# Kernel optimization log

Measured on AMD Instinct MI355X. Metric: run time of the kernel, lower is better.

Reference implementation:

```python
import jax, jax.numpy as jnp
import numpy as np

INC, OUTC, NHEADS, KSIZE = 256, 256, 8, 5


def setup_inputs() -> dict:
    key = jax.random.key(0)
    k1, k2 = jax.random.split(key, 2)
    x = jax.random.normal(k1, (4, INC, 64, 64), dtype=jnp.float32)
    w_qkv = jax.random.normal(k2, (3 * OUTC, INC), dtype=jnp.float32) * 0.02
    b_qkv = jnp.zeros((3 * OUTC,), dtype=jnp.float32)
    return {"x": x, "w_qkv": w_qkv, "b_qkv": b_qkv}


def reference(x, w_qkv, b_qkv):
    N, Cin, H, W = x.shape
    hd = OUTC // NHEADS
    ofs = KSIZE // 2
    K2 = KSIZE * KSIZE

    # 1x1 conv == pointwise matmul over channels
    qkv = jnp.einsum('nchw,dc->ndhw', x, w_qkv) + b_qkv[None, :, None, None]
    Q = qkv[:, :OUTC]
    K = qkv[:, OUTC:2 * OUTC]
    V = qkv[:, 2 * OUTC:]

    # Zero-pad K/V; track validity so boundary softmax only spans in-bounds
    # positions (the torch code slices smaller windows at borders -> no pad
    # contribution to softmax).
    Kp = jnp.pad(K, ((0, 0), (0, 0), (ofs, ofs), (ofs, ofs)))
    Vp = jnp.pad(V, ((0, 0), (0, 0), (ofs, ofs), (ofs, ofs)))
    valid = jnp.pad(jnp.ones((H, W), dtype=bool), ((ofs, ofs), (ofs, ofs)))

    # Sliding windows via KSIZE^2 static shifted slices: [N,D,H,W,K2]
    k_win = jnp.stack([Kp[:, :, dy:dy + H, dx:dx + W]
                       for dy in range(KSIZE) for dx in range(KSIZE)], axis=-1)
    v_win = jnp.stack([Vp[:, :, dy:dy + H, dx:dx + W]
                       for dy in range(KSIZE) for dx in range(KSIZE)], axis=-1)
    m_win = jnp.stack([valid[dy:dy + H, dx:dx + W]
                       for dy in range(KSIZE) for dx in range(KSIZE)], axis=-1)  # [H,W,K2]

    qh = Q.reshape(N, NHEADS, hd, H, W)
    kh = k_win.reshape(N, NHEADS, hd, H, W, K2)
    vh = v_win.reshape(N, NHEADS, hd, H, W, K2)

    scores = jnp.einsum('ngdhw,ngdhwk->nghwk', qh, kh)          # [N,G,H,W,K2]
    scores = jnp.where(m_win[None, None], scores, -jnp.inf)
    att = jax.nn.softmax(scores, axis=-1)
    out = jnp.einsum('nghwk,ngdhwk->ngdhw', att, vh)            # [N,G,hd,H,W]
    return out.reshape(N, OUTC, H, W)
```

## Files before the change

kernel.cpp:

```cpp
#include <hip/hip_runtime.h>
#include <hip/hip_bf16.h>
#include <math.h>

#define CIN 256
#define COUT 768
#define OUTC 256
#define HH 64
#define WW 64
#define HW 4096

typedef unsigned int uint32;
typedef unsigned short ushort16;

using short8 = __attribute__((ext_vector_type(8))) short;
using f32x4  = __attribute__((ext_vector_type(4))) float;

__device__ inline uint32 pkbf2(float a, float b) {
    __hip_bfloat162 h = __float22bfloat162_rn(make_float2(a, b));
    union { __hip_bfloat162 h2; uint32 u; } cv; cv.h2 = h;
    return cv.u;
}
__device__ inline uint32 pkhf2(float a, float b) {
    union { _Float16 h[2]; uint32 u; } cv;
    cv.h[0] = (_Float16)a; cv.h[1] = (_Float16)b;
    return cv.u;
}
__device__ inline float f16lo(uint32 u) {
    union { uint32 u; _Float16 h[2]; } c; c.u = u; return (float)c.h[0];
}
__device__ inline float f16hi(uint32 u) {
    union { uint32 u; _Float16 h[2]; } c; c.u = u; return (float)c.h[1];
}
__device__ inline float dpp_xor1(float x) {
#if __has_builtin(__builtin_amdgcn_update_dpp)
    int i = __builtin_amdgcn_update_dpp(0, __float_as_int(x),
                                        0xB1, 0xF, 0xF, true);
    return __int_as_float(i);
#else
    return __shfl_xor(x, 1, 64);
#endif
}

__global__ __launch_bounds__(256) void qkv_gemm_kernel(
    const float* __restrict__ x, const float* __restrict__ wq,
    const float* __restrict__ bq, ushort16* __restrict__ qkv)
{
    __shared__ uint4 As[512];
    __shared__ uint4 Bs[256];

    const int n   = blockIdx.z;
    const int d0  = blockIdx.y * 128;
    const int p0  = blockIdx.x * 64;
    const int tid = threadIdx.x;
    const int lane = tid & 63;
    const int wid  = tid >> 6;
    const int wm = wid >> 1;
    const int wn = wid & 1;

    const int ar = tid >> 1;
    const int ac0 = (tid & 1) * 2;
    const float* aptr = wq + (size_t)(d0 + ar) * CIN + ac0 * 8;
    const int pp = (tid & 31) * 2;
    const int kq = (tid >> 5) * 4;
    const int bchunk = kq >> 3;
    const int bsub   = (kq >> 2) & 1;
    const float* bptr = x + (size_t)n * CIN * HW + (size_t)kq * HW + p0 + pp;

    const int lrow = lane & 15;
    const int kc   = lane >> 4;

    f32x4 acc[4][2];
    #pragma unroll
    for (int i = 0; i < 4; ++i)
        #pragma unroll
        for (int j = 0; j < 2; ++j) acc[i][j] = (f32x4){0.f, 0.f, 0.f, 0.f};

    float4 a_st[4];
    float2 b_st[4];

    {
        a_st[0] = *(const float4*)(aptr);
        a_st[1] = *(const float4*)(aptr + 4);
        a_st[2] = *(const float4*)(aptr + 8);
        a_st[3] = *(const float4*)(aptr + 12);
        #pragma unroll
        for (int j = 0; j < 4; ++j)
            b_st[j] = *(const float2*)(bptr + (size_t)j * HW);
    }

    const int au0 = (ar * 4 + ac0)     ^ (ar & 7);
    const int au1 = (ar * 4 + ac0 + 1) ^ (ar & 7);
    const int bx  = (pp >> 1) & 7;
    const int bu0 = (pp * 4 + bchunk)       ^ bx;
    const int bu1 = ((pp + 1) * 4 + bchunk) ^ bx;

    #pragma unroll 1
    for (int kt = 0; kt < 8; ++kt) {
        __syncthreads();

        As[au0] = make_uint4(pkbf2(a_st[0].x, a_st[0].y), pkbf2(a_st[0].z, a_st[0].w),
                             pkbf2(a_st[1].x, a_st[1].y), pkbf2(a_st[1].z, a_st[1].w));
        As[au1] = make_uint4(pkbf2(a_st[2].x, a_st[2].y), pkbf2(a_st[2].z, a_st[2].w),
                             pkbf2(a_st[3].x, a_st[3].y), pkbf2(a_st[3].z, a_st[3].w));
        {
            uint2 v0 = make_uint2(pkbf2(b_st[0].x, b_st[1].x), pkbf2(b_st[2].x, b_st[3].x));
            uint2 v1 = make_uint2(pkbf2(b_st[0].y, b_st[1].y), pkbf2(b_st[2].y, b_st[3].y));
            ((uint2*)&Bs[bu0])[bsub] = v0;
            ((uint2*)&Bs[bu1])[bsub] = v1;
        }

        if (kt < 7) {
            const int ko = (kt + 1) * 32;
            a_st[0] = *(const float4*)(aptr + ko);
            a_st[1] = *(const float4*)(aptr + ko + 4);
            a_st[2] = *(const float4*)(aptr + ko + 8);
            a_st[3] = *(const float4*)(aptr + ko + 12);
            #pragma unroll
            for (int j = 0; j < 4; ++j)
                b_st[j] = *(const float2*)(bptr + (size_t)(ko + j) * HW);
        }

        __syncthreads();

        short8 af[4], bf[2];
        #pragma unroll
        for (int fm = 0; fm < 4; ++fm) {
            const int r = wm * 64 + fm * 16 + lrow;
            af[fm] = *(const short8*)&As[(r * 4 + kc) ^ (r & 7)];
        }
        #pragma unroll
        for (int fn = 0; fn < 2; ++fn) {
            const int p = wn * 32 + fn * 16 + lrow;
            bf[fn] = *(const short8*)&Bs[(p * 4 + kc) ^ ((p >> 1) & 7)];
        }
        #pragma unroll
        for (int fm = 0; fm < 4; ++fm)
            #pragma unroll
            for (int fn = 0; fn < 2; ++fn)
                acc[fm][fn] = __builtin_amdgcn_mfma_f32_16x16x32_bf16(
                    af[fm], bf[fn], acc[fm][fn], 0, 0, 0);
    }

    const int hi4 = lane >> 4;
    ushort16* qn = qkv + (size_t)n * COUT * HW;
    #pragma unroll
    for (int fm = 0; fm < 4; ++fm) {
        const int D = d0 + wm * 64 + fm * 16 + hi4 * 4;
        const float4 bias = *(const float4*)(&bq[D]);
        const int slot = D >> 5, dlow = D & 31;
        ushort16* qs = qn + (size_t)slot * (HW * 32) + dlow;
        #pragma unroll
        for (int fn = 0; fn < 2; ++fn) {
            const int p = p0 + wn * 32 + fn * 16 + lrow;
            f32x4 v = acc[fm][fn];
            uint32 u0 = pkhf2(v[0] + bias.x, v[1] + bias.y);
            uint32 u1 = pkhf2(v[2] + bias.z, v[3] + bias.w);
            *(uint2*)(qs + (size_t)p * 32) = make_uint2(u0, u1);
        }
    }
}

#define TR 4
#define TC 32
#define HR 8
#define HC 36
#define NPIX (HR*HC)

__global__ __launch_bounds__(256) void attn_kernel(
    const ushort16* __restrict__ qkv, float* __restrict__ out)
{
    __shared__ uint4 Ks[NPIX * 4];
    __shared__ uint4 Vs[NPIX * 4];

    const int n    = blockIdx.z;
    const int head = blockIdx.y;
    const int ht = blockIdx.x >> 1;
    const int wt = blockIdx.x & 1;
    const int h0 = ht * TR;
    const int w0 = wt * TC;

    const int tid  = threadIdx.x;
    const int half = tid & 1;
    const int wc   = (tid >> 1) & 31;
    const int tr   = tid >> 6;

    const int h = h0 + tr, w = w0 + wc;
    const int p = h * WW + w;

    const uint4* Kb = (const uint4*)(qkv + ((size_t)(n * 24 + 8 + head)) * HW * 32);
    const uint4* Vb = (const uint4*)(qkv + ((size_t)(n * 24 + 16 + head)) * HW * 32);

    for (int c = tid; c < 2 * NPIX * 4; c += 256) {
        const int b  = (c >= NPIX * 4);
        const int cc = c - b * NPIX * 4;
        const int pix = cc >> 2, i = cc & 3;
        const int hr = pix / HC, cw = pix - hr * HC;
        const int hh = h0 + hr - 2, ww = w0 + cw - 2;
        if (hh >= 0 && hh < HH && ww >= 0 && ww < WW) {
            const int pp = hh * WW + ww;
            const uint4 v = (b ? Vb : Kb)[(size_t)pp * 4 + i];
            const int unit = (pix * 4 + i) ^ (pix & 7);
            (b ? Vs : Ks)[unit] = v;
        }
    }

    float qf[16];
    {
        const uint4* Qp = (const uint4*)(qkv + (((size_t)(n * 24 + head)) * HW + p) * 32);
        #pragma unroll
        for (int i = 0; i < 2; ++i) {
            uint4 u = Qp[half * 2 + i];
            qf[8*i+0] = f16lo(u.x); qf[8*i+1] = f16hi(u.x);
            qf[8*i+2] = f16lo(u.y); qf[8*i+3] = f16hi(u.y);
            qf[8*i+4] = f16lo(u.z); qf[8*i+5] = f16hi(u.z);
            qf[8*i+6] = f16lo(u.w); qf[8*i+7] = f16hi(u.w);
        }
    }

    __syncthreads();

    float sc[25];
    #pragma unroll
    for (int ky = 0; ky < 5; ++ky) {
        const int hh = h + ky - 2;
        const int hr = tr + ky;
        #pragma unroll
        for (int kx = 0; kx < 5; ++kx) {
            const int ww = w + kx - 2;
            float s;
            if (hh >= 0 && hh < HH && ww >= 0 && ww < WW) {
                const int pix = hr * HC + (wc + kx);
                const int u0 = (pix * 4 + half * 2)     ^ (pix & 7);
                const int u1 = (pix * 4 + half * 2 + 1) ^ (pix & 7);
                uint4 a = Ks[u0], b = Ks[u1];
                float t = 0.f;
                t = fmaf(qf[0],  f16lo(a.x), t); t = fmaf(qf[1],  f16hi(a.x), t);
                t = fmaf(qf[2],  f16lo(a.y), t); t = fmaf(qf[3],  f16hi(a.y), t);
                t = fmaf(qf[4],  f16lo(a.z), t); t = fmaf(qf[5],  f16hi(a.z), t);
                t = fmaf(qf[6],  f16lo(a.w), t); t = fmaf(qf[7],  f16hi(a.w), t);
                t = fmaf(qf[8],  f16lo(b.x), t); t = fmaf(qf[9],  f16hi(b.x), t);
                t = fmaf(qf[10], f16lo(b.y), t); t = fmaf(qf[11], f16hi(b.y), t);
                t = fmaf(qf[12], f16lo(b.z), t); t = fmaf(qf[13], f16hi(b.z), t);
                t = fmaf(qf[14], f16lo(b.w), t); t = fmaf(qf[15], f16hi(b.w), t);
                s = t;
            } else {
                s = -1e30f;
            }
            sc[ky * 5 + kx] = s;
        }
    }
    #pragma unroll
    for (int k = 0; k < 25; ++k) {
        float o = dpp_xor1(sc[k]);
        sc[k] = (sc[k] <= -1e29f) ? sc[k] : sc[k] + o;
    }

    float m = sc[0];
    #pragma unroll
    for (int k = 1; k < 25; ++k) m = fmaxf(m, sc[k]);
    float sum = 0.f;
    #pragma unroll
    for (int k = 0; k < 25; ++k) {
        float e = __expf(sc[k] - m);
        sc[k] = e;
        sum += e;
    }
    const float inv = 1.f / sum;

    float al[8], ah[8];
    #pragma unroll
    for (int i = 0; i < 8; ++i) { al[i] = 0.f; ah[i] = 0.f; }
    #pragma unroll
    for (int ky = 0; ky < 5; ++ky) {
        const int hh = h + ky - 2;
        if (hh < 0 || hh >= HH) continue;
        const int hr = tr + ky;
        #pragma unroll
        for (int kx = 0; kx < 5; ++kx) {
            const int ww = w + kx - 2;
            if (ww < 0 || ww >= WW) continue;
            const float a = sc[ky * 5 + kx];
            const int pix = hr * HC + (wc + kx);
            const int u0 = (pix * 4 + half * 2)     ^ (pix & 7);
            const int u1 = (pix * 4 + half * 2 + 1) ^ (pix & 7);
            uint4 xv = Vs[u0], yv = Vs[u1];
            al[0] = fmaf(a, f16lo(xv.x), al[0]); ah[0] = fmaf(a, f16hi(xv.x), ah[0]);
            al[1] = fmaf(a, f16lo(xv.y), al[1]); ah[1] = fmaf(a, f16hi(xv.y), ah[1]);
            al[2] = fmaf(a, f16lo(xv.z), al[2]); ah[2] = fmaf(a, f16hi(xv.z), ah[2]);
            al[3] = fmaf(a, f16lo(xv.w), al[3]); ah[3] = fmaf(a, f16hi(xv.w), ah[3]);
            al[4] = fmaf(a, f16lo(yv.x), al[4]); ah[4] = fmaf(a, f16hi(yv.x), ah[4]);
            al[5] = fmaf(a, f16lo(yv.y), al[5]); ah[5] = fmaf(a, f16hi(yv.y), ah[5]);
            al[6] = fmaf(a, f16lo(yv.z), al[6]); ah[6] = fmaf(a, f16hi(yv.z), ah[6]);
            al[7] = fmaf(a, f16lo(yv.w), al[7]); ah[7] = fmaf(a, f16hi(yv.w), ah[7]);
        }
    }

    float* Ob = out + ((size_t)(n * 8 + head) * 32 + half * 16) * HW + p;
    #pragma unroll
    for (int i = 0; i < 8; ++i) {
        Ob[(size_t)(2*i)   * HW] = al[i] * inv;
        Ob[(size_t)(2*i+1) * HW] = ah[i] * inv;
    }
}

extern "C" void kernel_launch(void* const* d_in, const int* in_sizes, int n_in,
                              void* d_out, int out_size, void* d_ws, size_t ws_size,
                              hipStream_t stream) {
    const float* x  = (const float*)d_in[0];
    const float* wq = (const float*)d_in[1];
    const float* bq = (const float*)d_in[2];
    float* out = (float*)d_out;
    ushort16* qkv = (ushort16*)d_ws;

    dim3 g1(HW / 64, COUT / 128, 4);
    qkv_gemm_kernel<<<g1, 256, 0, stream>>>(x, wq, bq, qkv);

    dim3 g2(32, 8, 4);
    attn_kernel<<<g2, 256, 0, stream>>>(qkv, out);
}
```

Measured before the change: 50.54 us.

## Enlarge QKV GEMM tile to 128x128 with two large K-stages in LDS

The QKV projection GEMM moves from a 128x64 output tile with 8 register-prefetched K steps of 32 to a 128x128 tile that stages K in two halves of 128 through 64KB of LDS, dropping the XOR swizzle for a k-chunk-major layout. Each wave now computes a 64x64 sub-tile (4x4 MFMAs), which raises operand reuse and halves the number of blocks and barriers. The cost is much larger LDS use and more accumulator registers, which lowers occupancy. The register prefetch that overlapped global loads with MFMA is also removed, so loads and compute now alternate in two exposed phases. The unswizzled LDS layout may also cause bank conflicts.

```diff
diff --git a/kernel.cpp b/kernel.cpp
--- a/kernel.cpp
+++ b/kernel.cpp
@@ -45,100 +45,84 @@
     const float* __restrict__ x, const float* __restrict__ wq,
     const float* __restrict__ bq, ushort16* __restrict__ qkv)
 {
-    __shared__ uint4 As[512];
-    __shared__ uint4 Bs[256];
+    __shared__ uint4 As[2048];
+    __shared__ uint4 Bs[2048];
 
     const int n   = blockIdx.z;
     const int d0  = blockIdx.y * 128;
-    const int p0  = blockIdx.x * 64;
+    const int p0  = blockIdx.x * 128;
     const int tid = threadIdx.x;
     const int lane = tid & 63;
     const int wid  = tid >> 6;
-    const int wm = wid >> 1;
-    const int wn = wid & 1;
-
-    const int ar = tid >> 1;
-    const int ac0 = (tid & 1) * 2;
-    const float* aptr = wq + (size_t)(d0 + ar) * CIN + ac0 * 8;
-    const int pp = (tid & 31) * 2;
-    const int kq = (tid >> 5) * 4;
-    const int bchunk = kq >> 3;
-    const int bsub   = (kq >> 2) & 1;
-    const float* bptr = x + (size_t)n * CIN * HW + (size_t)kq * HW + p0 + pp;
-
+    const int wm = wid >> 1, wn = wid & 1;
     const int lrow = lane & 15;
     const int kc   = lane >> 4;
 
-    f32x4 acc[4][2];
+    const int ar  = tid >> 1;
+    const int akh = tid & 1;
+    const int bp = tid & 127;
+    const int bg = tid >> 7;
+
+    const float* xb = x + (size_t)n * CIN * HW;
+
+    f32x4 acc[4][4];
     #pragma unroll
     for (int i = 0; i < 4; ++i)
         #pragma unroll
-        for (int j = 0; j < 2; ++j) acc[i][j] = (f32x4){0.f, 0.f, 0.f, 0.f};
-
-    float4 a_st[4];
-    float2 b_st[4];
-
-    {
-        a_st[0] = *(const float4*)(aptr);
-        a_st[1] = *(const float4*)(aptr + 4);
-        a_st[2] = *(const float4*)(aptr + 8);
-        a_st[3] = *(const float4*)(aptr + 12);
-        #pragma unroll
-        for (int j = 0; j < 4; ++j)
-            b_st[j] = *(const float2*)(bptr + (size_t)j * HW);
-    }
-
-    const int au0 = (ar * 4 + ac0)     ^ (ar & 7);
-    const int au1 = (ar * 4 + ac0 + 1) ^ (ar & 7);
-    const int bx  = (pp >> 1) & 7;
-    const int bu0 = (pp * 4 + bchunk)       ^ bx;
-    const int bu1 = ((pp + 1) * 4 + bchunk) ^ bx;
-
-    #pragma unroll 1
-    for (int kt = 0; kt < 8; ++kt) {
+        for (int j = 0; j < 4; ++j) acc[i][j] = (f32x4){0.f, 0.f, 0.f, 0.f};
+
+    #pragma unroll
+    for (int kh = 0; kh < 2; ++kh) {
+        const int k0 = kh * 128;
+        if (kh) __syncthreads();
+
+        {
+            const float* ap = wq + (size_t)(d0 + ar) * CIN + k0 + akh * 64;
+            #pragma unroll
+            for (int j = 0; j < 8; ++j) {
+                float4 v0 = *(const float4*)(ap + j * 8);
+                float4 v1 = *(const float4*)(ap + j * 8 + 4);
+                As[(akh * 8 + j) * 128 + ar] =
+                    make_uint4(pkbf2(v0.x, v0.y), pkbf2(v0.z, v0.w),
+                               pkbf2(v1.x, v1.y), pkbf2(v1.z, v1.w));
+            }
+        }
+        {
+            const float* bptr = xb + (size_t)(k0 + bg * 64) * HW + p0 + bp;
+            #pragma unroll
+            for (int j = 0; j < 8; ++j) {
+                float c0 = bptr[(size_t)(j * 8 + 0) * HW];
+                float c1 = bptr[(size_t)(j * 8 + 1) * HW];
+                float c2 = bptr[(size_t)(j * 8 + 2) * HW];
+                float c3 = bptr[(size_t)(j * 8 + 3) * HW];
+                float c4 = bptr[(size_t)(j * 8 + 4) * HW];
+                float c5 = bptr[(size_t)(j * 8 + 5) * HW];
+                float c6 = bptr[(size_t)(j * 8 + 6) * HW];
+                float c7 = bptr[(size_t)(j * 8 + 7) * HW];
+                Bs[(bg * 8 + j) * 128 + bp] =
+                    make_uint4(pkbf2(c0, c1), pkbf2(c2, c3),
+                               pkbf2(c4, c5), pkbf2(c6, c7));
+            }
+        }
+
         __syncthreads();
 
-        As[au0] = make_uint4(pkbf2(a_st[0].x, a_st[0].y), pkbf2(a_st[0].z, a_st[0].w),
-                             pkbf2(a_st[1].x, a_st[1].y), pkbf2(a_st[1].z, a_st[1].w));
-        As[au1] = make_uint4(pkbf2(a_st[2].x, a_st[2].y), pkbf2(a_st[2].z, a_st[2].w),
-                             pkbf2(a_st[3].x, a_st[3].y), pkbf2(a_st[3].z, a_st[3].w));
-        {
-            uint2 v0 = make_uint2(pkbf2(b_st[0].x, b_st[1].x), pkbf2(b_st[2].x, b_st[3].x));
-            uint2 v1 = make_uint2(pkbf2(b_st[0].y, b_st[1].y), pkbf2(b_st[2].y, b_st[3].y));
-            ((uint2*)&Bs[bu0])[bsub] = v0;
-            ((uint2*)&Bs[bu1])[bsub] = v1;
-        }
-
-        if (kt < 7) {
-            const int ko = (kt + 1) * 32;
-            a_st[0] = *(const float4*)(aptr + ko);
-            a_st[1] = *(const float4*)(aptr + ko + 4);
-            a_st[2] = *(const float4*)(aptr + ko + 8);
-            a_st[3] = *(const float4*)(aptr + ko + 12);
-            #pragma unroll
-            for (int j = 0; j < 4; ++j)
-                b_st[j] = *(const float2*)(bptr + (size_t)(ko + j) * HW);
-        }
-
-        __syncthreads();
-
-        short8 af[4], bf[2];
-        #pragma unroll
-        for (int fm = 0; fm < 4; ++fm) {
-            const int r = wm * 64 + fm * 16 + lrow;
-            af[fm] = *(const short8*)&As[(r * 4 + kc) ^ (r & 7)];
-        }
-        #pragma unroll
-        for (int fn = 0; fn < 2; ++fn) {
-            const int p = wn * 32 + fn * 16 + lrow;
-            bf[fn] = *(const short8*)&Bs[(p * 4 + kc) ^ ((p >> 1) & 7)];
-        }
-        #pragma unroll
-        for (int fm = 0; fm < 4; ++fm)
-            #pragma unroll
-            for (int fn = 0; fn < 2; ++fn)
-                acc[fm][fn] = __builtin_amdgcn_mfma_f32_16x16x32_bf16(
-                    af[fm], bf[fn], acc[fm][fn], 0, 0, 0);
+        #pragma unroll
+        for (int kt = 0; kt < 4; ++kt) {
+            short8 af[4], bf[4];
+            #pragma unroll
+            for (int fm = 0; fm < 4; ++fm)
+                af[fm] = *(const short8*)&As[(kt * 4 + kc) * 128 + wm * 64 + fm * 16 + lrow];
+            #pragma unroll
+            for (int fn = 0; fn < 4; ++fn)
+                bf[fn] = *(const short8*)&Bs[(kt * 4 + kc) * 128 + wn * 64 + fn * 16 + lrow];
+            #pragma unroll
+            for (int fm = 0; fm < 4; ++fm)
+                #pragma unroll
+                for (int fn = 0; fn < 4; ++fn)
+                    acc[fm][fn] = __builtin_amdgcn_mfma_f32_16x16x32_bf16(
+                        af[fm], bf[fn], acc[fm][fn], 0, 0, 0);
+        }
     }
 
     const int hi4 = lane >> 4;
@@ -150,8 +134,8 @@
         const int slot = D >> 5, dlow = D & 31;
         ushort16* qs = qn + (size_t)slot * (HW * 32) + dlow;
         #pragma unroll
-        for (int fn = 0; fn < 2; ++fn) {
-            const int p = p0 + wn * 32 + fn * 16 + lrow;
+        for (int fn = 0; fn < 4; ++fn) {
+            const int p = p0 + wn * 64 + fn * 16 + lrow;
             f32x4 v = acc[fm][fn];
             uint32 u0 = pkhf2(v[0] + bias.x, v[1] + bias.y);
             uint32 u1 = pkhf2(v[2] + bias.z, v[3] + bias.w);
@@ -312,7 +296,7 @@
     float* out = (float*)d_out;
     ushort16* qkv = (ushort16*)d_ws;
 
-    dim3 g1(HW / 64, COUT / 128, 4);
+    dim3 g1(HW / 128, COUT / 128, 4);
     qkv_gemm_kernel<<<g1, 256, 0, stream>>>(x, wq, bq, qkv);
 
     dim3 g2(32, 8, 4);
```

Measured after the change: 51.98 us. +2.8%, slower.
